# Kernel optimization log

Hardware: AMD Instinct MI355X
Metric: run time of the kernel (lower is better)

## Reference

```python
import jax, jax.numpy as jnp
import numpy as np
from math import sqrt

B, L, S, H, E, D = 4, 2048, 2048, 16, 64, 64


def setup_inputs() -> dict:
    key = jax.random.key(0)
    kq, kk, kv = jax.random.split(key, 3)
    queries = jax.random.normal(kq, (B, L, H, E), dtype=jnp.float32)
    keys = jax.random.normal(kk, (B, S, H, E), dtype=jnp.float32)
    values = jax.random.normal(kv, (B, S, H, D), dtype=jnp.float32)
    # TriangularCausalMask: True above the diagonal (positions to mask out)
    attn_mask = jnp.broadcast_to(
        jnp.triu(jnp.ones((L, S), dtype=bool), k=1)[None, None], (B, 1, L, S)
    )
    return {"queries": queries, "keys": keys, "values": values, "attn_mask": attn_mask}


def reference(queries, keys, values, attn_mask):
    # B, L, H, E = queries.shape ; scale = 1/sqrt(E) (self.scale is None)
    scale = 1.0 / sqrt(queries.shape[-1])
    # scores: [B, H, L, S]
    scores = jnp.einsum("blhe,bshe->bhls", queries, keys)
    # mask_flag=True: masked_fill with -inf before scaling (scale*(-inf) = -inf)
    scores = jnp.where(attn_mask, -jnp.inf, scores)
    A = jax.nn.softmax(scale * scores, axis=-1)  # dropout p=0.0 -> identity
    V = jnp.einsum("bhls,bshd->blhd", A, values)
    return V
```

## Files before the change

kernel.cpp:

```cpp
#include <hip/hip_runtime.h>
#include <hip/hip_bf16.h>

typedef __bf16 bf16x8 __attribute__((ext_vector_type(8)));
typedef float floatx4 __attribute__((ext_vector_type(4)));

#define Bc 4
#define Lc 2048
#define Sc 2048
#define Hc 16
#define Ec 64
#define Dc 64
#define QB 128
#define NQTB (Lc/QB)
#define NPAIRB (NQTB/2)

__device__ __forceinline__ bf16x8 pack8f(const float* f){
  bf16x8 r;
  #pragma unroll
  for (int i=0;i<8;++i) r[i] = (__bf16)f[i];
  return r;
}

template<int CTRL>
__device__ __forceinline__ float dppf(float x){
  return __builtin_bit_cast(float,
    __builtin_amdgcn_update_dpp(0, __builtin_bit_cast(int, x), CTRL, 0xF, 0xF, true));
}
__device__ __forceinline__ float rowmax16(float x){
  x = fmaxf(x, dppf<0xB1>(x));
  x = fmaxf(x, dppf<0x4E>(x));
  x = fmaxf(x, dppf<0x141>(x));
  x = fmaxf(x, dppf<0x140>(x));
  return x;
}
__device__ __forceinline__ float rowsum16(float x){
  x += dppf<0xB1>(x);
  x += dppf<0x4E>(x);
  x += dppf<0x141>(x);
  x += dppf<0x140>(x);
  return x;
}

__global__ __launch_bounds__(256)
void fa_fwd(const float* __restrict__ Q, const float* __restrict__ K,
            const float* __restrict__ V, float* __restrict__ O)
{
  int nid = blockIdx.x;
  int bid = (nid & 7) * ((int)gridDim.x >> 3) + (nid >> 3);
  int pid = bid & (NPAIRB - 1);
  int h  = (bid >> 3) & (Hc - 1);
  int b  = bid >> 7;

  int tid  = threadIdx.x;
  int w    = tid >> 6;
  int lane = tid & 63;
  int lg   = lane >> 4;
  int lr   = lane & 15;

  __shared__ __align__(16) char Kl[2][64*128];
  __shared__ __align__(16) char Vl[2][64*128];
  __shared__ __align__(16) char Pl[4][16*64*2];
  char* Pw = Pl[w];

  const int skr = tid >> 2, seg = tid & 3;
  const int sd  = tid & 63, skb = tid >> 6;
  const unsigned xk = (skr & 7) << 4;
  const unsigned xv = (sd  & 7) << 4;

  const float* Kb = K + ((size_t)(b*Sc)*Hc + h)*Ec;
  const float* Vb = V + ((size_t)(b*Sc)*Hc + h)*Dc;

  float kf[16], vf[16];

  #pragma unroll 1
  for (int pass=0; pass<2; ++pass) {
    const int qtb = pass ? (NQTB-1-pid) : pid;
    const int q0w = qtb*QB + w*32;

    bf16x8 aq[2][2];
    #pragma unroll
    for (int s2=0; s2<2; ++s2) {
      const float* qp = Q + ((size_t)(b*Lc + q0w + s2*16 + lr)*Hc + h)*Ec;
      float tmp[8];
      #pragma unroll
      for (int c=0; c<2; ++c) {
        *(float4*)(tmp)   = *(const float4*)(qp + c*32 + lg*8);
        *(float4*)(tmp+4) = *(const float4*)(qp + c*32 + lg*8 + 4);
        #pragma unroll
        for (int i=0;i<8;++i) tmp[i] *= 0.125f;
        aq[s2][c] = pack8f(tmp);
      }
    }

    floatx4 o[2][4];
    float m[2][4], lsum[2][4];
    #pragma unroll
    for (int s2=0; s2<2; ++s2)
      #pragma unroll
      for (int i=0;i<4;++i){ o[s2][i] = (floatx4){0.f,0.f,0.f,0.f}; m[s2][i] = -3.0e38f; lsum[s2][i] = 0.f; }

    {
      const float* ks = Kb + (size_t)skr*Hc*Ec + seg*16;
      *(float4*)(kf)    = *(const float4*)(ks);
      *(float4*)(kf+4)  = *(const float4*)(ks+4);
      *(float4*)(kf+8)  = *(const float4*)(ks+8);
      *(float4*)(kf+12) = *(const float4*)(ks+12);
      const float* vs = Vb + (size_t)(skb*16)*Hc*Dc + sd;
      #pragma unroll
      for (int i=0;i<16;++i) vf[i] = vs[(size_t)i*Hc*Dc];
    }

    const int nt = 2*qtb + 2;
    for (int t = 0; t < nt; ++t) {
      char* Kcur = Kl[t&1];
      char* Vcur = Vl[t&1];

      *(bf16x8*)(Kcur + skr*128 + ((seg*32)      ^ xk)) = pack8f(kf);
      *(bf16x8*)(Kcur + skr*128 + ((seg*32 + 16) ^ xk)) = pack8f(kf+8);
      *(bf16x8*)(Vcur + sd*128  + ((skb*32)      ^ xv)) = pack8f(vf);
      *(bf16x8*)(Vcur + sd*128  + ((skb*32 + 16) ^ xv)) = pack8f(vf+8);
      __syncthreads();

      if (t+1 < nt) {
        const float* ks = Kb + (size_t)((t+1)*64 + skr)*Hc*Ec + seg*16;
        *(float4*)(kf)    = *(const float4*)(ks);
        *(float4*)(kf+4)  = *(const float4*)(ks+4);
        *(float4*)(kf+8)  = *(const float4*)(ks+8);
        *(float4*)(kf+12) = *(const float4*)(ks+12);
        const float* vs = Vb + (size_t)((t+1)*64 + skb*16)*Hc*Dc + sd;
        #pragma unroll
        for (int i=0;i<16;++i) vf[i] = vs[(size_t)i*Hc*Dc];
      }

      if (t*64 <= q0w + 31) {
        const int t64 = t*64;
        const bool needmask = (t64 + 63 > q0w);

        #pragma unroll
        for (int s2=0; s2<2; ++s2) {
          floatx4 s[4];
          #pragma unroll
          for (int nf=0; nf<4; ++nf) {
            int kr = nf*16 + lr;
            unsigned xr = (kr & 7) << 4;
            const char* kp = Kcur + kr*128;
            bf16x8 b0 = *(const bf16x8*)(kp + ((lg*16)      ^ xr));
            bf16x8 b1 = *(const bf16x8*)(kp + ((64 + lg*16) ^ xr));
            floatx4 acc = (floatx4){0.f,0.f,0.f,0.f};
            acc = __builtin_amdgcn_mfma_f32_16x16x32_bf16(aq[s2][0], b0, acc, 0, 0, 0);
            acc = __builtin_amdgcn_mfma_f32_16x16x32_bf16(aq[s2][1], b1, acc, 0, 0, 0);
            s[nf] = acc;
          }

          if (needmask) {
            const int qq = q0w + s2*16 + lg*4;
            #pragma unroll
            for (int nf=0; nf<4; ++nf)
              #pragma unroll
              for (int r=0; r<4; ++r)
                if (t64 + nf*16 + lr > qq + r) s[nf][r] = -3.0e38f;
          }

          float mx[4], rs[4], al[4];
          #pragma unroll
          for (int r=0;r<4;++r) {
            mx[r] = rowmax16(fmaxf(fmaxf(s[0][r], s[1][r]), fmaxf(s[2][r], s[3][r])));
            float mn = fmaxf(m[s2][r], mx[r]);
            al[r] = __expf(m[s2][r] - mn);
            m[s2][r] = mn;
            rs[r] = 0.f;
          }
          #pragma unroll
          for (int nf=0; nf<4; ++nf)
            #pragma unroll
            for (int r=0;r<4;++r) {
              float p = __expf(s[nf][r] - m[s2][r]);
              rs[r] += p;
              s[nf][r] = p;
            }
          #pragma unroll
          for (int r=0;r<4;++r) {
            rs[r] = rowsum16(rs[r]);
            lsum[s2][r] = lsum[s2][r]*al[r] + rs[r];
          }
          #pragma unroll
          for (int df=0; df<4; ++df)
            #pragma unroll
            for (int r=0;r<4;++r) o[s2][df][r] *= al[r];

          #pragma unroll
          for (int nf=0; nf<4; ++nf)
            #pragma unroll
            for (int r=0;r<4;++r) {
              int q = lg*4 + r;
              int k = nf*16 + lr;
              *(__bf16*)(Pw + q*128 + ((k*2) ^ ((q&7)<<4))) = (__bf16)s[nf][r];
            }

          {
            unsigned xq = (lr & 7) << 4;
            const char* pp = Pw + lr*128;
            bf16x8 pa0 = *(const bf16x8*)(pp + ((lg*16)      ^ xq));
            bf16x8 pa1 = *(const bf16x8*)(pp + ((64 + lg*16) ^ xq));
            #pragma unroll
            for (int df=0; df<4; ++df) {
              int d = df*16 + lr;
              unsigned xd = (d & 7) << 4;
              const char* vp = Vcur + d*128;
              bf16x8 vb0 = *(const bf16x8*)(vp + ((lg*16)      ^ xd));
              bf16x8 vb1 = *(const bf16x8*)(vp + ((64 + lg*16) ^ xd));
              o[s2][df] = __builtin_amdgcn_mfma_f32_16x16x32_bf16(pa0, vb0, o[s2][df], 0, 0, 0);
              o[s2][df] = __builtin_amdgcn_mfma_f32_16x16x32_bf16(pa1, vb1, o[s2][df], 0, 0, 0);
            }
          }
        }
      }
      __syncthreads();
    }

    #pragma unroll
    for (int s2=0; s2<2; ++s2)
      #pragma unroll
      for (int r=0;r<4;++r) {
        float inv = 1.0f / lsum[s2][r];
        int qg = q0w + s2*16 + lg*4 + r;
        float* op = O + ((size_t)(b*Lc + qg)*Hc + h)*Dc;
        #pragma unroll
        for (int df=0; df<4; ++df)
          op[df*16 + lr] = o[s2][df][r] * inv;
      }
  }
}

extern "C" void kernel_launch(void* const* d_in, const int* in_sizes, int n_in,
                              void* d_out, int out_size, void* d_ws, size_t ws_size,
                              hipStream_t stream) {
  const float* Q = (const float*)d_in[0];
  const float* K = (const float*)d_in[1];
  const float* V = (const float*)d_in[2];
  float* O = (float*)d_out;
  dim3 grid(Bc * Hc * NPAIRB);
  dim3 block(256);
  fa_fwd<<<grid, block, 0, stream>>>(Q, K, V, O);
}
```

Before: 120.1 us.

## Pre-convert K/V to swizzled bf16 tiles and stream them via global_load_lds

```diff
diff --git a/kernel.cpp b/kernel.cpp
--- a/kernel.cpp
+++ b/kernel.cpp
@@ -3,6 +3,7 @@
 
 typedef __bf16 bf16x8 __attribute__((ext_vector_type(8)));
 typedef float floatx4 __attribute__((ext_vector_type(4)));
+typedef unsigned int u32;
 
 #define Bc 4
 #define Lc 2048
@@ -10,9 +11,12 @@
 #define Hc 16
 #define Ec 64
 #define Dc 64
-#define QB 128
-#define NQTB (Lc/QB)
-#define NPAIRB (NQTB/2)
+#define NQT (Lc/64)
+#define NPAIR (NQT/2)
+#define NT (Sc/64)
+#define TILEB 8192
+#define WSK ((size_t)Bc*Hc*NT*TILEB)
+#define WSNEED (2*WSK)
 
 __device__ __forceinline__ bf16x8 pack8f(const float* f){
   bf16x8 r;
@@ -41,9 +45,207 @@
   return x;
 }
 
+__device__ __forceinline__ void gload16(const void* g, void* l){
+  __builtin_amdgcn_global_load_lds(
+      (const __attribute__((address_space(1))) u32*)g,
+      (__attribute__((address_space(3))) u32*)l, 16, 0, 0);
+}
+
 __global__ __launch_bounds__(256)
-void fa_fwd(const float* __restrict__ Q, const float* __restrict__ K,
-            const float* __restrict__ V, float* __restrict__ O)
+void prep(const float* __restrict__ K, const float* __restrict__ V,
+          char* __restrict__ ws)
+{
+  const int t = blockIdx.x*256 + threadIdx.x;
+  if (t < (1<<20)) {
+    const int c = t & 7, r = (t>>3) & 63, tile = (t>>9) & 31, h = (t>>14) & 15, b = t>>18;
+    const float* src = K + ((size_t)((b*Sc + tile*64 + r))*Hc + h)*Ec + c*8;
+    float tmp[8];
+    *(float4*)(tmp)   = *(const float4*)(src);
+    *(float4*)(tmp+4) = *(const float4*)(src + 4);
+    char* dst = ws + (size_t)((b*Hc + h)*NT + tile)*TILEB + r*128 + ((c ^ (r&7))<<4);
+    *(bf16x8*)dst = pack8f(tmp);
+  } else {
+    const int u = t - (1<<20);
+    const int d = u & 63, c = (u>>6) & 7, tile = (u>>9) & 31, h = (u>>14) & 15, b = u>>18;
+    const float* src = V + ((size_t)((b*Sc + tile*64 + c*8))*Hc + h)*Dc + d;
+    bf16x8 v;
+    #pragma unroll
+    for (int kk=0; kk<8; ++kk) v[kk] = (__bf16)src[(size_t)kk*Hc*Dc];
+    char* dst = ws + WSK + (size_t)((b*Hc + h)*NT + tile)*TILEB + d*128 + ((c ^ (d&7))<<4);
+    *(bf16x8*)dst = v;
+  }
+}
+
+__global__ __launch_bounds__(256)
+void fa_fwd(const float* __restrict__ Q, const char* __restrict__ ws,
+            float* __restrict__ O)
+{
+  int nid = blockIdx.x;
+  int bid = (nid & 7) * ((int)gridDim.x >> 3) + (nid >> 3);
+  int pid = bid & (NPAIR - 1);
+  int h  = (bid >> 4) & (Hc - 1);
+  int b  = bid >> 8;
+
+  int tid  = threadIdx.x;
+  int w    = tid >> 6;
+  int lane = tid & 63;
+  int lg   = lane >> 4;
+  int lr   = lane & 15;
+
+  __shared__ __align__(16) char Kl[2][64*128];
+  __shared__ __align__(16) char Vl[2][64*128];
+  __shared__ __align__(16) char Pl[4][16*64*2];
+  char* Pw = Pl[w];
+
+  const char* gK = ws +        (size_t)((b*Hc + h)*NT)*TILEB;
+  const char* gV = ws + WSK +  (size_t)((b*Hc + h)*NT)*TILEB;
+  const int soff = w*2048 + lane*16;
+
+  #pragma unroll 1
+  for (int pass=0; pass<2; ++pass) {
+    const int qt = pass ? (NQT-1-pid) : pid;
+
+    const int qrow = qt*64 + w*16 + lr;
+    const float* qp = Q + ((size_t)(b*Lc + qrow)*Hc + h)*Ec;
+    bf16x8 aq[2];
+    {
+      float tmp[8];
+      #pragma unroll
+      for (int c=0; c<2; ++c) {
+        *(float4*)(tmp)   = *(const float4*)(qp + c*32 + lg*8);
+        *(float4*)(tmp+4) = *(const float4*)(qp + c*32 + lg*8 + 4);
+        #pragma unroll
+        for (int i=0;i<8;++i) tmp[i] *= 0.125f;
+        aq[c] = pack8f(tmp);
+      }
+    }
+
+    floatx4 o[4];
+    float m[4], lsum[4];
+    #pragma unroll
+    for (int i=0;i<4;++i){ o[i] = (floatx4){0.f,0.f,0.f,0.f}; m[i] = -3.0e38f; lsum[i] = 0.f; }
+
+    {
+      const char* sK = gK + soff;
+      const char* sV = gV + soff;
+      gload16(sK,        &Kl[0][w*2048]);
+      gload16(sK + 1024, &Kl[0][w*2048 + 1024]);
+      gload16(sV,        &Vl[0][w*2048]);
+      gload16(sV + 1024, &Vl[0][w*2048 + 1024]);
+    }
+    __syncthreads();
+
+    const int nt = qt + 1;
+    for (int t = 0; t < nt; ++t) {
+      char* Kcur = Kl[t&1];
+      char* Vcur = Vl[t&1];
+
+      if (t+1 < nt) {
+        const int nb = (t+1)&1;
+        const char* sK = gK + (size_t)(t+1)*TILEB + soff;
+        const char* sV = gV + (size_t)(t+1)*TILEB + soff;
+        gload16(sK,        &Kl[nb][w*2048]);
+        gload16(sK + 1024, &Kl[nb][w*2048 + 1024]);
+        gload16(sV,        &Vl[nb][w*2048]);
+        gload16(sV + 1024, &Vl[nb][w*2048 + 1024]);
+      }
+
+      floatx4 s[4];
+      #pragma unroll
+      for (int nf=0; nf<4; ++nf) {
+        int kr = nf*16 + lr;
+        unsigned xr = (kr & 7) << 4;
+        const char* kp = Kcur + kr*128;
+        bf16x8 b0 = *(const bf16x8*)(kp + ((lg*16)      ^ xr));
+        bf16x8 b1 = *(const bf16x8*)(kp + ((64 + lg*16) ^ xr));
+        floatx4 acc = (floatx4){0.f,0.f,0.f,0.f};
+        acc = __builtin_amdgcn_mfma_f32_16x16x32_bf16(aq[0], b0, acc, 0, 0, 0);
+        acc = __builtin_amdgcn_mfma_f32_16x16x32_bf16(aq[1], b1, acc, 0, 0, 0);
+        s[nf] = acc;
+      }
+
+      if (t == qt) {
+        #pragma unroll
+        for (int nf=0; nf<4; ++nf)
+          #pragma unroll
+          for (int r=0; r<4; ++r)
+            if (nf*16 + lr > w*16 + lg*4 + r) s[nf][r] = -3.0e38f;
+      }
+
+      float mx[4], rs[4], al[4];
+      #pragma unroll
+      for (int r=0;r<4;++r) {
+        mx[r] = rowmax16(fmaxf(fmaxf(s[0][r], s[1][r]), fmaxf(s[2][r], s[3][r])));
+        float mn = fmaxf(m[r], mx[r]);
+        al[r] = __expf(m[r] - mn);
+        m[r] = mn;
+        rs[r] = 0.f;
+      }
+      #pragma unroll
+      for (int nf=0; nf<4; ++nf)
+        #pragma unroll
+        for (int r=0;r<4;++r) {
+          float p = __expf(s[nf][r] - m[r]);
+          rs[r] += p;
+          s[nf][r] = p;
+        }
+      #pragma unroll
+      for (int r=0;r<4;++r) {
+        rs[r] = rowsum16(rs[r]);
+        lsum[r] = lsum[r]*al[r] + rs[r];
+      }
+      #pragma unroll
+      for (int df=0; df<4; ++df)
+        #pragma unroll
+        for (int r=0;r<4;++r) o[df][r] *= al[r];
+
+      #pragma unroll
+      for (int nf=0; nf<4; ++nf)
+        #pragma unroll
+        for (int r=0;r<4;++r) {
+          int q = lg*4 + r;
+          int k = nf*16 + lr;
+          *(__bf16*)(Pw + q*128 + ((k*2) ^ ((q&7)<<4))) = (__bf16)s[nf][r];
+        }
+
+      {
+        unsigned xq = (lr & 7) << 4;
+        const char* pp = Pw + lr*128;
+        bf16x8 pa0 = *(const bf16x8*)(pp + ((lg*16)      ^ xq));
+        bf16x8 pa1 = *(const bf16x8*)(pp + ((64 + lg*16) ^ xq));
+        #pragma unroll
+        for (int df=0; df<4; ++df) {
+          int d = df*16 + lr;
+          unsigned xd = (d & 7) << 4;
+          const char* vp = Vcur + d*128;
+          bf16x8 vb0 = *(const bf16x8*)(vp + ((lg*16)      ^ xd));
+          bf16x8 vb1 = *(const bf16x8*)(vp + ((64 + lg*16) ^ xd));
+          o[df] = __builtin_amdgcn_mfma_f32_16x16x32_bf16(pa0, vb0, o[df], 0, 0, 0);
+          o[df] = __builtin_amdgcn_mfma_f32_16x16x32_bf16(pa1, vb1, o[df], 0, 0, 0);
+        }
+      }
+      __syncthreads();
+    }
+
+    #pragma unroll
+    for (int r=0;r<4;++r) {
+      float inv = 1.0f / lsum[r];
+      int qg = qt*64 + w*16 + lg*4 + r;
+      float* op = O + ((size_t)(b*Lc + qg)*Hc + h)*Dc;
+      #pragma unroll
+      for (int df=0; df<4; ++df)
+        op[df*16 + lr] = o[df][r] * inv;
+    }
+  }
+}
+
+#define QB 128
+#define NQTB (Lc/QB)
+#define NPAIRB (NQTB/2)
+
+__global__ __launch_bounds__(256)
+void fa_fwd_fb(const float* __restrict__ Q, const float* __restrict__ K,
+               const float* __restrict__ V, float* __restrict__ O)
 {
   int nid = blockIdx.x;
   int bid = (nid & 7) * ((int)gridDim.x >> 3) + (nid >> 3);
@@ -239,7 +441,12 @@
   const float* K = (const float*)d_in[1];
   const float* V = (const float*)d_in[2];
   float* O = (float*)d_out;
-  dim3 grid(Bc * Hc * NPAIRB);
-  dim3 block(256);
-  fa_fwd<<<grid, block, 0, stream>>>(Q, K, V, O);
-}
+
+  if (ws_size >= WSNEED) {
+    char* ws = (char*)d_ws;
+    prep<<<dim3((2u<<20)/256), dim3(256), 0, stream>>>(K, V, ws);
+    fa_fwd<<<dim3(Bc * Hc * NPAIR), dim3(256), 0, stream>>>(Q, ws, O);
+  } else {
+    fa_fwd_fb<<<dim3(Bc * Hc * NPAIRB), dim3(256), 0, stream>>>(Q, K, V, O);
+  }
+}
```

After: 111.7 us. 1.08x faster.
